# Kernel optimization log

Measured on AMD Instinct MI355X. Metric: run time of the kernel, lower is better.

The kernel has to match this reference:

```python
import jax, jax.numpy as jnp
import numpy as np

T, B, H, V, L = 512, 8, 256, 32000, 3
THRESH = 1.0

# Heaviside spike with ATan surrogate gradient (snntorch default, alpha=2)
@jax.custom_vjp
def spike(u):
    return (u > 0).astype(u.dtype)

def _spike_fwd(u):
    return (u > 0).astype(u.dtype), u

def _spike_bwd(u, g):
    return (g / (1.0 + (jnp.pi * u) ** 2),)

spike.defvjp(_spike_fwd, _spike_bwd)


def leaky_scan(cur, beta):
    """mem[t] = beta * mem[t-1] + cur[t]; cur: (T,B,H), beta: (H,). No reset -> associative."""
    def step(mem, c):
        mem = beta * mem + c
        return mem, mem
    _, mems = jax.lax.scan(step, jnp.zeros(cur.shape[1:], cur.dtype), cur)
    return mems  # (T,B,H)


def setup_inputs() -> dict:
    key = jax.random.key(0)
    ks = jax.random.split(key, 10)
    s = 1.0 / np.sqrt(H)
    return {
        "tokens": jax.random.randint(ks[0], (T, B), 0, V),
        "token_emb": jax.random.normal(ks[1], (V, H), dtype=jnp.float32) * 0.02,
        "pos_emb": jax.random.normal(ks[2], (T, H), dtype=jnp.float32) * 0.02,
        "Wq": jax.random.normal(ks[3], (L, H, H), dtype=jnp.float32) * s,
        "bq": jnp.zeros((L, H), dtype=jnp.float32),
        "beta": jax.random.uniform(ks[4], (L, H), minval=0.5, maxval=0.95),
        "Wfc": jax.random.normal(ks[5], (L, H, H), dtype=jnp.float32) * s,
        "bfc": jnp.zeros((L, H), dtype=jnp.float32),
        "Wout": jax.random.normal(ks[6], (H, V), dtype=jnp.float32) * s,
        "bout": jnp.zeros((V,), dtype=jnp.float32),
    }


def reference(tokens, token_emb, pos_emb, Wq, bq, beta, Wfc, bfc, Wout, bout):
    # embed: (T,B,H) + broadcast positional (T,1,H)
    h = token_emb[tokens] + pos_emb[:, None, :]
    for l in range(L):  # small fixed layer count
        cur = jnp.einsum('tbh,hd->tbd', h, Wq[l]) + bq[l]   # q-projection
        mem = leaky_scan(cur, beta[l])                       # leaky integrate, no reset
        spk = spike(mem - THRESH)                            # heaviside spikes
        h = jax.nn.relu(jnp.einsum('tbh,hd->tbd', spk, Wfc[l]) + bfc[l])
    logits = jnp.einsum('tbh,hv->tbv', h, Wout) + bout       # (T,B,V)
    return logits
```

## Files before the change

kernel.cpp:

```cpp
#include <hip/hip_runtime.h>
#include <hip/hip_bf16.h>
#include <cstddef>

constexpr int T_ = 512;
constexpr int B_ = 8;
constexpr int H_ = 256;
constexpr int V_ = 32000;
constexpr int L_ = 3;
constexpr int M_ = T_ * B_;

typedef __attribute__((ext_vector_type(8))) short short8;
typedef __attribute__((ext_vector_type(4))) float floatx4;

__device__ __forceinline__ unsigned short f2bf(float f) {
    unsigned u = __float_as_uint(f);
    u += 0x7fffu + ((u >> 16) & 1u);
    return (unsigned short)(u >> 16);
}

__device__ __forceinline__ void gl_lds16(const void* g, void* l) {
    __builtin_amdgcn_global_load_lds((__attribute__((address_space(1))) void*)g,
                                     (__attribute__((address_space(3))) void*)l,
                                     16, 0, 0);
}

__global__ __launch_bounds__(256) void embed_kernel(
    const int* __restrict__ tokens, const float* __restrict__ temb,
    const float* __restrict__ pemb, unsigned short* __restrict__ hb)
{
    const int idx = blockIdx.x * 256 + threadIdx.x;
    const int h4 = idx & (H_ / 4 - 1);
    const int tb = idx >> 6;
    const int b  = tb & (B_ - 1);
    const int t  = tb >> 3;
    const int tok = tokens[t * B_ + b];
    const float4 e = *(const float4*)&temb[(size_t)tok * H_ + h4 * 4];
    const float4 p = *(const float4*)&pemb[(size_t)t * H_ + h4 * 4];
    ushort4 r;
    r.x = f2bf(e.x + p.x); r.y = f2bf(e.y + p.y);
    r.z = f2bf(e.z + p.z); r.w = f2bf(e.w + p.w);
    *(ushort4*)&hb[(size_t)idx * 4] = r;
}

constexpr int CH_ = 32;
constexpr int NT_ = T_ / CH_;
constexpr int TS_ = B_ * H_;

__global__ __launch_bounds__(256) void scan_local_kernel(
    const float* __restrict__ cur, const float* __restrict__ beta_l,
    float* __restrict__ mloc)
{
    const int c = blockIdx.x, b = blockIdx.y, h = threadIdx.x;
    const float bt = beta_l[h];
    const size_t off = ((size_t)(c * CH_) * B_ + b) * H_ + h;
    const float* p = cur + off;
    float* q = mloc + off;
    float mem = 0.0f;
    #pragma unroll
    for (int tt = 0; tt < CH_; ++tt) {
        mem = fmaf(bt, mem, p[(size_t)tt * TS_]);
        q[(size_t)tt * TS_] = mem;
    }
}

__global__ __launch_bounds__(256) void scan_apply_kernel(
    const float* __restrict__ mloc, const float* __restrict__ beta_l,
    unsigned short* __restrict__ spk)
{
    const int c = blockIdx.x, b = blockIdx.y, h = threadIdx.x;
    const float bt = beta_l[h];
    float b32 = bt;
    #pragma unroll
    for (int i = 0; i < 5; ++i) b32 *= b32;
    float carry = 0.0f;
    for (int j = 0; j < c; ++j)
        carry = fmaf(b32, carry,
                     mloc[((size_t)(j * CH_ + CH_ - 1) * B_ + b) * H_ + h]);
    const size_t off = ((size_t)(c * CH_) * B_ + b) * H_ + h;
    const float* p = mloc + off;
    unsigned short* q = spk + off;
    float pw = bt;
    #pragma unroll
    for (int tt = 0; tt < CH_; ++tt) {
        const float mem = fmaf(pw, carry, p[(size_t)tt * TS_]);
        pw *= bt;
        q[(size_t)tt * TS_] = (mem > 1.0f) ? (unsigned short)0x3F80u
                                           : (unsigned short)0u;
    }
}

__global__ __launch_bounds__(256) void transpose_small_kernel(
    const float* __restrict__ Wq, const float* __restrict__ Wfc,
    unsigned short* __restrict__ WT)
{
    __shared__ float t[64][65];
    const int z = blockIdx.z;
    const float* src = (z < 3) ? Wq + (size_t)z * H_ * H_
                               : Wfc + (size_t)(z - 3) * H_ * H_;
    unsigned short* dst = WT + (size_t)z * H_ * H_;
    const int n0 = blockIdx.x * 64, k0 = blockIdx.y * 64;
    const int x = threadIdx.x & 63, y = threadIdx.x >> 6;
    #pragma unroll
    for (int i = 0; i < 16; ++i)
        t[y + 4 * i][x] = src[(size_t)(k0 + y + 4 * i) * H_ + n0 + x];
    __syncthreads();
    #pragma unroll
    for (int i = 0; i < 16; ++i)
        dst[(size_t)(n0 + y + 4 * i) * H_ + k0 + x] = f2bf(t[x][y + 4 * i]);
}

__global__ __launch_bounds__(256) void transpose_wout_kernel(
    const float* __restrict__ W, unsigned short* __restrict__ Wt)
{
    __shared__ float t[64][65];
    const int n0 = blockIdx.x * 64;
    const int k0 = blockIdx.y * 64;
    const int x = threadIdx.x & 63, y = threadIdx.x >> 6;
    #pragma unroll
    for (int i = 0; i < 16; ++i)
        t[y + 4 * i][x] = W[(size_t)(k0 + y + 4 * i) * V_ + n0 + x];
    __syncthreads();
    #pragma unroll
    for (int i = 0; i < 16; ++i)
        Wt[(size_t)(n0 + y + 4 * i) * H_ + k0 + x] = f2bf(t[x][y + 4 * i]);
}


__global__ __launch_bounds__(256, 2) void gemm_mfma_out(
    const unsigned short* __restrict__ A,
    const unsigned short* __restrict__ Bt,
    const float* __restrict__ bias,
    float* __restrict__ C)
{
    constexpr int K = H_, N = V_;
    __shared__ __align__(16) short lA[2048][8];
    __shared__ __align__(16) short lB[1024][8];

    const int tid = threadIdx.x;
    const int lane = tid & 63, wave = tid >> 6;
    const int wm = wave >> 1, wn = wave & 1;
    const int l15 = lane & 15, quad = lane >> 4;
    const int m0 = blockIdx.x * 256;
    const int n0 = blockIdx.y * 128;

    floatx4 acc[8][4] = {};

    for (int k0 = 0; k0 < K; k0 += 64) {
        #pragma unroll
        for (int j = 0; j < 8; ++j) {
            const int base = (wave * 8 + j) * 64;
            const int s = base + lane;
            const int row = s >> 3;
            const int oct = (s & 7) ^ (row & 7);
            gl_lds16(A + (size_t)(m0 + row) * K + k0 + oct * 8, &lA[base][0]);
        }
        #pragma unroll
        for (int j = 0; j < 4; ++j) {
            const int base = (wave * 4 + j) * 64;
            const int s = base + lane;
            const int row = s >> 3;
            const int oct = (s & 7) ^ (row & 7);
            gl_lds16(Bt + (size_t)(n0 + row) * K + k0 + oct * 8, &lB[base][0]);
        }
        __syncthreads();

        #pragma unroll
        for (int t = 0; t < 2; ++t) {
            short8 af[8], bf[4];
            #pragma unroll
            for (int f = 0; f < 8; ++f) {
                const int ra = wm * 128 + f * 16 + l15;
                af[f] = *(const short8*)&lA[ra * 8 + ((4 * t + quad) ^ (ra & 7))][0];
            }
            #pragma unroll
            for (int g = 0; g < 4; ++g) {
                const int rb = wn * 64 + g * 16 + l15;
                bf[g] = *(const short8*)&lB[rb * 8 + ((4 * t + quad) ^ (rb & 7))][0];
            }
            #pragma unroll
            for (int f = 0; f < 8; ++f)
                #pragma unroll
                for (int g = 0; g < 4; ++g)
                    acc[f][g] = __builtin_amdgcn_mfma_f32_16x16x32_bf16(
                        af[f], bf[g], acc[f][g], 0, 0, 0);
        }
        __syncthreads();
    }

    float* scr = (float*)&lA[0][0] + (size_t)wave * 1088;
    float bvv[4];
    #pragma unroll
    for (int g = 0; g < 4; ++g)
        bvv[g] = bias[n0 + wn * 64 + g * 16 + l15];

    #pragma unroll
    for (int f = 0; f < 8; ++f) {
        #pragma unroll
        for (int g = 0; g < 4; ++g)
            #pragma unroll
            for (int r = 0; r < 4; ++r)
                scr[(quad * 4 + r) * 68 + g * 16 + l15] = acc[f][g][r] + bvv[g];
        __syncthreads();
        #pragma unroll
        for (int rr = 0; rr < 4; ++rr) {
            const int ml = rr * 4 + quad;
            const floatx4 v = *(const floatx4*)&scr[ml * 68 + l15 * 4];
            const size_t m = (size_t)(m0 + wm * 128 + f * 16 + ml);
            __builtin_nontemporal_store(
                v, (floatx4*)&C[m * (size_t)N + n0 + wn * 64 + l15 * 4]);
        }
        __syncthreads();
    }
}

template <int RELU, int OUT_BF16>
__global__ __launch_bounds__(256) void gemm_mfma_layer(
    const unsigned short* __restrict__ A,
    const unsigned short* __restrict__ Bt,
    const float* __restrict__ bias,
    float* __restrict__ Cf, unsigned short* __restrict__ Cb)
{
    constexpr int K = H_, N = H_;
    __shared__ __align__(16) short lA[1024][8];
    __shared__ __align__(16) short lB[512][8];

    const int tid = threadIdx.x;
    const int lane = tid & 63, wave = tid >> 6;
    const int wm = wave >> 1, wn = wave & 1;
    const int l15 = lane & 15, quad = lane >> 4;
    const int m0 = blockIdx.x * 128;
    const int n0 = blockIdx.y * 64;

    floatx4 acc[4][2] = {};

    for (int k0 = 0; k0 < K; k0 += 64) {
        #pragma unroll
        for (int j = 0; j < 4; ++j) {
            const int base = (wave * 4 + j) * 64;
            const int s = base + lane;
            const int row = s >> 3;
            const int oct = (s & 7) ^ (row & 7);
            gl_lds16(A + (size_t)(m0 + row) * K + k0 + oct * 8, &lA[base][0]);
        }
        #pragma unroll
        for (int j = 0; j < 2; ++j) {
            const int base = (wave * 2 + j) * 64;
            const int s = base + lane;
            const int row = s >> 3;
            const int oct = (s & 7) ^ (row & 7);
            gl_lds16(Bt + (size_t)(n0 + row) * K + k0 + oct * 8, &lB[base][0]);
        }
        __syncthreads();

        #pragma unroll
        for (int t = 0; t < 2; ++t) {
            short8 af[4], bf[2];
            #pragma unroll
            for (int f = 0; f < 4; ++f) {
                const int ra = wm * 64 + f * 16 + l15;
                af[f] = *(const short8*)&lA[ra * 8 + ((4 * t + quad) ^ (ra & 7))][0];
            }
            #pragma unroll
            for (int f = 0; f < 2; ++f) {
                const int rb = wn * 32 + f * 16 + l15;
                bf[f] = *(const short8*)&lB[rb * 8 + ((4 * t + quad) ^ (rb & 7))][0];
            }
            #pragma unroll
            for (int i = 0; i < 4; ++i)
                #pragma unroll
                for (int j2 = 0; j2 < 2; ++j2)
                    acc[i][j2] = __builtin_amdgcn_mfma_f32_16x16x32_bf16(
                        af[i], bf[j2], acc[i][j2], 0, 0, 0);
        }
        __syncthreads();
    }

    #pragma unroll
    for (int j2 = 0; j2 < 2; ++j2) {
        const int col = n0 + wn * 32 + j2 * 16 + l15;
        const float bv = bias[col];
        #pragma unroll
        for (int i = 0; i < 4; ++i) {
            const int rbase = m0 + wm * 64 + i * 16 + quad * 4;
            #pragma unroll
            for (int r = 0; r < 4; ++r) {
                float v = acc[i][j2][r] + bv;
                if (RELU) v = fmaxf(v, 0.0f);
                if (OUT_BF16)
                    Cb[(size_t)(rbase + r) * N + col] = f2bf(v);
                else
                    Cf[(size_t)(rbase + r) * N + col] = v;
            }
        }
    }
}

extern "C" void kernel_launch(void* const* d_in, const int* in_sizes, int n_in,
                              void* d_out, int out_size, void* d_ws, size_t ws_size,
                              hipStream_t stream)
{
    const int*   tokens = (const int*)  d_in[0];
    const float* temb   = (const float*)d_in[1];
    const float* pemb   = (const float*)d_in[2];
    const float* Wq     = (const float*)d_in[3];
    const float* bq     = (const float*)d_in[4];
    const float* beta   = (const float*)d_in[5];
    const float* Wfc    = (const float*)d_in[6];
    const float* bfc    = (const float*)d_in[7];
    const float* Wout   = (const float*)d_in[8];
    const float* bout   = (const float*)d_in[9];
    float* out = (float*)d_out;

    unsigned short* h_bf  = (unsigned short*)d_ws;
    unsigned short* spk   = h_bf + (size_t)M_ * H_;
    unsigned short* WT    = spk + (size_t)M_ * H_;
    unsigned short* WoutT = WT + (size_t)2 * L_ * H_ * H_;
    float*          cur   = (float*)(WoutT + (size_t)V_ * H_);
    float*          mloc  = cur + (size_t)M_ * H_;

    transpose_small_kernel<<<dim3(4, 4, 6), 256, 0, stream>>>(Wq, Wfc, WT);
    transpose_wout_kernel<<<dim3(V_ / 64, H_ / 64), 256, 0, stream>>>(Wout, WoutT);

    embed_kernel<<<(M_ * H_ / 4) / 256, 256, 0, stream>>>(tokens, temb, pemb, h_bf);

    for (int l = 0; l < L_; ++l) {
        const unsigned short* WqT  = WT + (size_t)l * H_ * H_;
        const unsigned short* WfcT = WT + (size_t)(L_ + l) * H_ * H_;
        gemm_mfma_layer<0, 0><<<dim3(M_ / 128, H_ / 64), 256, 0, stream>>>(
            h_bf, WqT, bq + (size_t)l * H_, cur, nullptr);
        scan_local_kernel<<<dim3(NT_, B_), 256, 0, stream>>>(
            cur, beta + (size_t)l * H_, mloc);
        scan_apply_kernel<<<dim3(NT_, B_), 256, 0, stream>>>(
            mloc, beta + (size_t)l * H_, spk);
        gemm_mfma_layer<1, 1><<<dim3(M_ / 128, H_ / 64), 256, 0, stream>>>(
            spk, WfcT, bfc + (size_t)l * H_, nullptr, h_bf);
    }

    gemm_mfma_out<<<dim3(M_ / 256, V_ / 128), 256, 0, stream>>>(
        h_bf, WoutT, bout, out);
}
```

Baseline: 657.0 us.

## Double-buffer output GEMM, merge weight transposes, shrink layer GEMM tiles

The output GEMM now walks K in 32-wide steps with two LDS buffers, prefetching the next slice while MFMAs run on the current one, and its swizzle is adjusted to the narrower rows. Its epilogue block barriers are replaced by per-wave LDS waitcnts, since each wave only touches its own scratch region. The two weight-transpose kernels are merged into a single launch, and the layer GEMMs use 64-row tiles so twice as many blocks run. The aim is to hide global-load latency, cut barrier and launch overhead, and raise occupancy, at the cost of more loop iterations and barriers in the main loop.

```diff
diff --git a/kernel.cpp b/kernel.cpp
--- a/kernel.cpp
+++ b/kernel.cpp
@@ -89,40 +89,36 @@
     }
 }
 
-__global__ __launch_bounds__(256) void transpose_small_kernel(
+__global__ __launch_bounds__(256) void transpose_all_kernel(
     const float* __restrict__ Wq, const float* __restrict__ Wfc,
-    unsigned short* __restrict__ WT)
+    const float* __restrict__ Wout,
+    unsigned short* __restrict__ WT, unsigned short* __restrict__ WoutT)
 {
     __shared__ float t[64][65];
-    const int z = blockIdx.z;
-    const float* src = (z < 3) ? Wq + (size_t)z * H_ * H_
-                               : Wfc + (size_t)(z - 3) * H_ * H_;
-    unsigned short* dst = WT + (size_t)z * H_ * H_;
-    const int n0 = blockIdx.x * 64, k0 = blockIdx.y * 64;
+    const int bx = blockIdx.x;
+    const float* src; unsigned short* dst;
+    int n0, k0, sstride;
+    if (bx < 96) {
+        const int z = bx >> 4, r = bx & 15;
+        src = (z < 3) ? Wq + (size_t)z * H_ * H_
+                      : Wfc + (size_t)(z - 3) * H_ * H_;
+        dst = WT + (size_t)z * H_ * H_;
+        n0 = (r & 3) * 64; k0 = (r >> 2) * 64;
+        sstride = H_;
+    } else {
+        const int nb = bx - 96;
+        src = Wout; dst = WoutT;
+        n0 = (nb >> 2) * 64; k0 = (nb & 3) * 64;
+        sstride = V_;
+    }
     const int x = threadIdx.x & 63, y = threadIdx.x >> 6;
     #pragma unroll
     for (int i = 0; i < 16; ++i)
-        t[y + 4 * i][x] = src[(size_t)(k0 + y + 4 * i) * H_ + n0 + x];
+        t[y + 4 * i][x] = src[(size_t)(k0 + y + 4 * i) * sstride + n0 + x];
     __syncthreads();
     #pragma unroll
     for (int i = 0; i < 16; ++i)
         dst[(size_t)(n0 + y + 4 * i) * H_ + k0 + x] = f2bf(t[x][y + 4 * i]);
-}
-
-__global__ __launch_bounds__(256) void transpose_wout_kernel(
-    const float* __restrict__ W, unsigned short* __restrict__ Wt)
-{
-    __shared__ float t[64][65];
-    const int n0 = blockIdx.x * 64;
-    const int k0 = blockIdx.y * 64;
-    const int x = threadIdx.x & 63, y = threadIdx.x >> 6;
-    #pragma unroll
-    for (int i = 0; i < 16; ++i)
-        t[y + 4 * i][x] = W[(size_t)(k0 + y + 4 * i) * V_ + n0 + x];
-    __syncthreads();
-    #pragma unroll
-    for (int i = 0; i < 16; ++i)
-        Wt[(size_t)(n0 + y + 4 * i) * H_ + k0 + x] = f2bf(t[x][y + 4 * i]);
 }
 
 
@@ -133,8 +129,8 @@
     float* __restrict__ C)
 {
     constexpr int K = H_, N = V_;
-    __shared__ __align__(16) short lA[2048][8];
-    __shared__ __align__(16) short lB[1024][8];
+    __shared__ __align__(16) short lA[2][1024][8];
+    __shared__ __align__(16) short lB[2][512][8];
 
     const int tid = threadIdx.x;
     const int lane = tid & 63, wave = tid >> 6;
@@ -145,49 +141,53 @@
 
     floatx4 acc[8][4] = {};
 
-    for (int k0 = 0; k0 < K; k0 += 64) {
-        #pragma unroll
-        for (int j = 0; j < 8; ++j) {
-            const int base = (wave * 8 + j) * 64;
-            const int s = base + lane;
-            const int row = s >> 3;
-            const int oct = (s & 7) ^ (row & 7);
-            gl_lds16(A + (size_t)(m0 + row) * K + k0 + oct * 8, &lA[base][0]);
-        }
+    auto stage = [&](int buf, int ks) {
+        const int k0 = ks * 32;
         #pragma unroll
         for (int j = 0; j < 4; ++j) {
             const int base = (wave * 4 + j) * 64;
             const int s = base + lane;
-            const int row = s >> 3;
-            const int oct = (s & 7) ^ (row & 7);
-            gl_lds16(Bt + (size_t)(n0 + row) * K + k0 + oct * 8, &lB[base][0]);
-        }
+            const int row = s >> 2;
+            const int oct = (s & 3) ^ ((row >> 1) & 3);
+            gl_lds16(A + (size_t)(m0 + row) * K + k0 + oct * 8, &lA[buf][base][0]);
+        }
+        #pragma unroll
+        for (int j = 0; j < 2; ++j) {
+            const int base = (wave * 2 + j) * 64;
+            const int s = base + lane;
+            const int row = s >> 2;
+            const int oct = (s & 3) ^ ((row >> 1) & 3);
+            gl_lds16(Bt + (size_t)(n0 + row) * K + k0 + oct * 8, &lB[buf][base][0]);
+        }
+    };
+
+    stage(0, 0);
+    __syncthreads();
+
+    for (int ks = 0; ks < 8; ++ks) {
+        const int cur = ks & 1;
+        if (ks < 7) stage(cur ^ 1, ks + 1);
+        short8 af[8], bf[4];
+        #pragma unroll
+        for (int f = 0; f < 8; ++f) {
+            const int ra = wm * 128 + f * 16 + l15;
+            af[f] = *(const short8*)&lA[cur][ra * 4 + (quad ^ ((ra >> 1) & 3))][0];
+        }
+        #pragma unroll
+        for (int g = 0; g < 4; ++g) {
+            const int rb = wn * 64 + g * 16 + l15;
+            bf[g] = *(const short8*)&lB[cur][rb * 4 + (quad ^ ((rb >> 1) & 3))][0];
+        }
+        #pragma unroll
+        for (int f = 0; f < 8; ++f)
+            #pragma unroll
+            for (int g = 0; g < 4; ++g)
+                acc[f][g] = __builtin_amdgcn_mfma_f32_16x16x32_bf16(
+                    af[f], bf[g], acc[f][g], 0, 0, 0);
         __syncthreads();
-
-        #pragma unroll
-        for (int t = 0; t < 2; ++t) {
-            short8 af[8], bf[4];
-            #pragma unroll
-            for (int f = 0; f < 8; ++f) {
-                const int ra = wm * 128 + f * 16 + l15;
-                af[f] = *(const short8*)&lA[ra * 8 + ((4 * t + quad) ^ (ra & 7))][0];
-            }
-            #pragma unroll
-            for (int g = 0; g < 4; ++g) {
-                const int rb = wn * 64 + g * 16 + l15;
-                bf[g] = *(const short8*)&lB[rb * 8 + ((4 * t + quad) ^ (rb & 7))][0];
-            }
-            #pragma unroll
-            for (int f = 0; f < 8; ++f)
-                #pragma unroll
-                for (int g = 0; g < 4; ++g)
-                    acc[f][g] = __builtin_amdgcn_mfma_f32_16x16x32_bf16(
-                        af[f], bf[g], acc[f][g], 0, 0, 0);
-        }
-        __syncthreads();
-    }
-
-    float* scr = (float*)&lA[0][0] + (size_t)wave * 1088;
+    }
+
+    float* scr = (float*)&lA[0][0][0] + (size_t)wave * 1088;
     float bvv[4];
     #pragma unroll
     for (int g = 0; g < 4; ++g)
@@ -200,7 +200,7 @@
             #pragma unroll
             for (int r = 0; r < 4; ++r)
                 scr[(quad * 4 + r) * 68 + g * 16 + l15] = acc[f][g][r] + bvv[g];
-        __syncthreads();
+        asm volatile("s_waitcnt lgkmcnt(0)" ::: "memory");
         #pragma unroll
         for (int rr = 0; rr < 4; ++rr) {
             const int ml = rr * 4 + quad;
@@ -209,7 +209,7 @@
             __builtin_nontemporal_store(
                 v, (floatx4*)&C[m * (size_t)N + n0 + wn * 64 + l15 * 4]);
         }
-        __syncthreads();
+        asm volatile("s_waitcnt lgkmcnt(0)" ::: "memory");
     }
 }
 
@@ -221,22 +221,22 @@
     float* __restrict__ Cf, unsigned short* __restrict__ Cb)
 {
     constexpr int K = H_, N = H_;
-    __shared__ __align__(16) short lA[1024][8];
+    __shared__ __align__(16) short lA[512][8];
     __shared__ __align__(16) short lB[512][8];
 
     const int tid = threadIdx.x;
     const int lane = tid & 63, wave = tid >> 6;
     const int wm = wave >> 1, wn = wave & 1;
     const int l15 = lane & 15, quad = lane >> 4;
-    const int m0 = blockIdx.x * 128;
+    const int m0 = blockIdx.x * 64;
     const int n0 = blockIdx.y * 64;
 
-    floatx4 acc[4][2] = {};
+    floatx4 acc[2][2] = {};
 
     for (int k0 = 0; k0 < K; k0 += 64) {
         #pragma unroll
-        for (int j = 0; j < 4; ++j) {
-            const int base = (wave * 4 + j) * 64;
+        for (int j = 0; j < 2; ++j) {
+            const int base = (wave * 2 + j) * 64;
             const int s = base + lane;
             const int row = s >> 3;
             const int oct = (s & 7) ^ (row & 7);
@@ -254,37 +254,37 @@
 
         #pragma unroll
         for (int t = 0; t < 2; ++t) {
-            short8 af[4], bf[2];
-            #pragma unroll
-            for (int f = 0; f < 4; ++f) {
-                const int ra = wm * 64 + f * 16 + l15;
+            short8 af[2], bf[2];
+            #pragma unroll
+            for (int f = 0; f < 2; ++f) {
+                const int ra = wm * 32 + f * 16 + l15;
                 af[f] = *(const short8*)&lA[ra * 8 + ((4 * t + quad) ^ (ra & 7))][0];
             }
             #pragma unroll
-            for (int f = 0; f < 2; ++f) {
-                const int rb = wn * 32 + f * 16 + l15;
-                bf[f] = *(const short8*)&lB[rb * 8 + ((4 * t + quad) ^ (rb & 7))][0];
+            for (int g = 0; g < 2; ++g) {
+                const int rb = wn * 32 + g * 16 + l15;
+                bf[g] = *(const short8*)&lB[rb * 8 + ((4 * t + quad) ^ (rb & 7))][0];
             }
             #pragma unroll
-            for (int i = 0; i < 4; ++i)
+            for (int f = 0; f < 2; ++f)
                 #pragma unroll
-                for (int j2 = 0; j2 < 2; ++j2)
-                    acc[i][j2] = __builtin_amdgcn_mfma_f32_16x16x32_bf16(
-                        af[i], bf[j2], acc[i][j2], 0, 0, 0);
+                for (int g = 0; g < 2; ++g)
+                    acc[f][g] = __builtin_amdgcn_mfma_f32_16x16x32_bf16(
+                        af[f], bf[g], acc[f][g], 0, 0, 0);
         }
         __syncthreads();
     }
 
     #pragma unroll
-    for (int j2 = 0; j2 < 2; ++j2) {
-        const int col = n0 + wn * 32 + j2 * 16 + l15;
+    for (int g = 0; g < 2; ++g) {
+        const int col = n0 + wn * 32 + g * 16 + l15;
         const float bv = bias[col];
         #pragma unroll
-        for (int i = 0; i < 4; ++i) {
-            const int rbase = m0 + wm * 64 + i * 16 + quad * 4;
+        for (int f = 0; f < 2; ++f) {
+            const int rbase = m0 + wm * 32 + f * 16 + quad * 4;
             #pragma unroll
             for (int r = 0; r < 4; ++r) {
-                float v = acc[i][j2][r] + bv;
+                float v = acc[f][g][r] + bv;
                 if (RELU) v = fmaxf(v, 0.0f);
                 if (OUT_BF16)
                     Cb[(size_t)(rbase + r) * N + col] = f2bf(v);
@@ -318,21 +318,21 @@
     float*          cur   = (float*)(WoutT + (size_t)V_ * H_);
     float*          mloc  = cur + (size_t)M_ * H_;
 
-    transpose_small_kernel<<<dim3(4, 4, 6), 256, 0, stream>>>(Wq, Wfc, WT);
-    transpose_wout_kernel<<<dim3(V_ / 64, H_ / 64), 256, 0, stream>>>(Wout, WoutT);
+    transpose_all_kernel<<<96 + (V_ / 64) * (H_ / 64), 256, 0, stream>>>(
+        Wq, Wfc, Wout, WT, WoutT);
 
     embed_kernel<<<(M_ * H_ / 4) / 256, 256, 0, stream>>>(tokens, temb, pemb, h_bf);
 
     for (int l = 0; l < L_; ++l) {
         const unsigned short* WqT  = WT + (size_t)l * H_ * H_;
         const unsigned short* WfcT = WT + (size_t)(L_ + l) * H_ * H_;
-        gemm_mfma_layer<0, 0><<<dim3(M_ / 128, H_ / 64), 256, 0, stream>>>(
+        gemm_mfma_layer<0, 0><<<dim3(M_ / 64, H_ / 64), 256, 0, stream>>>(
             h_bf, WqT, bq + (size_t)l * H_, cur, nullptr);
         scan_local_kernel<<<dim3(NT_, B_), 256, 0, stream>>>(
             cur, beta + (size_t)l * H_, mloc);
         scan_apply_kernel<<<dim3(NT_, B_), 256, 0, stream>>>(
             mloc, beta + (size_t)l * H_, spk);
-        gemm_mfma_layer<1, 1><<<dim3(M_ / 128, H_ / 64), 256, 0, stream>>>(
+        gemm_mfma_layer<1, 1><<<dim3(M_ / 64, H_ / 64), 256, 0, stream>>>(
             spk, WfcT, bfc + (size_t)l * H_, nullptr, h_bf);
     }
 
```

Result: no change. 661.0 us (+0.6%).
